# Kernel optimization log

Measured on AMD Instinct MI355X. Metric: run time of the kernel, lower is better.

The kernel has to match this reference:

```python
import jax, jax.numpy as jnp
import numpy as np

N, E, D, H, C = 20000, 320000, 128, 4, 128
NEG_SLOPE = 0.2

def _ln(x, g, b, eps=1e-5):
    mu = x.mean(-1, keepdims=True)
    var = ((x - mu) ** 2).mean(-1, keepdims=True)
    return (x - mu) * jax.lax.rsqrt(var + eps) * g + b

def _gatv2(x, src, dst, Wl, bl, Wr, br, att, b):
    # PyG GATv2Conv, concat=False (mean over heads), dropout off (eval)
    n = x.shape[0]
    xl = (x @ Wl + bl).reshape(n, H, C)   # source transform
    xr = (x @ Wr + br).reshape(n, H, C)   # destination transform
    e = jax.nn.leaky_relu(xl[src] + xr[dst], NEG_SLOPE)      # [E,H,C]
    score = jnp.einsum('ehc,hc->eh', e, att)                 # [E,H]
    m = jax.ops.segment_max(score, dst, num_segments=n)      # per-dst max
    w = jnp.exp(score - m[dst])
    denom = jax.ops.segment_sum(w, dst, num_segments=n)
    alpha = w / (denom[dst] + 1e-16)                         # softmax over incoming edges
    out = jax.ops.segment_sum(alpha[:, :, None] * xl[src], dst, num_segments=n)  # [N,H,C]
    return out.mean(axis=1) + b

def setup_inputs() -> dict:
    key = jax.random.key(0)
    ks = jax.random.split(key, 34)
    s = 1.0 / np.sqrt(D)
    def w(k, shape):
        return jax.random.normal(k, shape, jnp.float32) * s
    inp = {
        'x': jax.random.normal(ks[0], (N, D), jnp.float32),
        'edge_index': jax.random.randint(ks[1], (2, E), 0, N, jnp.int32),
        'W_in': w(ks[2], (D, C)), 'b_in': jnp.zeros((C,), jnp.float32),
        'c1_Wl': w(ks[3], (C, H * C)), 'c1_bl': jnp.zeros((H * C,), jnp.float32),
        'c1_Wr': w(ks[4], (C, H * C)), 'c1_br': jnp.zeros((H * C,), jnp.float32),
        'c1_att': w(ks[5], (H, C)), 'c1_b': jnp.zeros((C,), jnp.float32),
        'ln1_g': jnp.ones((C,), jnp.float32), 'ln1_b': jnp.zeros((C,), jnp.float32),
        'a_Wl': w(ks[6], (C, H * C)), 'a_bl': jnp.zeros((H * C,), jnp.float32),
        'a_Wr': w(ks[7], (C, H * C)), 'a_br': jnp.zeros((H * C,), jnp.float32),
        'a_att': w(ks[8], (H, C)), 'a_b': jnp.zeros((C,), jnp.float32),
        'aln_g': jnp.ones((C,), jnp.float32), 'aln_b': jnp.zeros((C,), jnp.float32),
        'ah_W': w(ks[9], (C, 1)), 'ah_b': jnp.zeros((1,), jnp.float32),
        'k_Wl': w(ks[10], (C, H * C)), 'k_bl': jnp.zeros((H * C,), jnp.float32),
        'k_Wr': w(ks[11], (C, H * C)), 'k_br': jnp.zeros((H * C,), jnp.float32),
        'k_att': w(ks[12], (H, C)), 'k_b': jnp.zeros((C,), jnp.float32),
        'kln_g': jnp.ones((C,), jnp.float32), 'kln_b': jnp.zeros((C,), jnp.float32),
        'kh_W': w(ks[13], (C, 1)), 'kh_b': jnp.zeros((1,), jnp.float32),
    }
    return inp

def reference(x, edge_index, W_in, b_in,
              c1_Wl, c1_bl, c1_Wr, c1_br, c1_att, c1_b, ln1_g, ln1_b,
              a_Wl, a_bl, a_Wr, a_br, a_att, a_b, aln_g, aln_b, ah_W, ah_b,
              k_Wl, k_bl, k_Wr, k_br, k_att, k_b, kln_g, kln_b, kh_W, kh_b):
    n = x.shape[0]
    loops = jnp.arange(n, dtype=edge_index.dtype)
    src = jnp.concatenate([edge_index[0], loops])  # PyG adds self-loops by default
    dst = jnp.concatenate([edge_index[1], loops])
    h = jax.nn.relu(x @ W_in + b_in)
    h_res = _gatv2(h, src, dst, c1_Wl, c1_bl, c1_Wr, c1_br, c1_att, c1_b)
    h = jax.nn.relu(_ln(h + h_res, ln1_g, ln1_b))
    xa = _gatv2(h, src, dst, a_Wl, a_bl, a_Wr, a_br, a_att, a_b)
    xa = jax.nn.relu(_ln(xa + h, aln_g, aln_b))
    action_logits = (xa @ ah_W + ah_b).squeeze(-1)
    xc = _gatv2(h, src, dst, k_Wl, k_bl, k_Wr, k_br, k_att, k_b)
    xc = jax.nn.relu(_ln(xc + h, kln_g, kln_b))
    state_value = xc @ kh_W + kh_b
    return action_logits, state_value
```

## Files before the change

### kernel.cpp

```cpp
#include <hip/hip_runtime.h>
#include <hip/hip_bf16.h>

typedef __hip_bfloat16 bf16;
typedef __attribute__((ext_vector_type(8))) short short8;
typedef __attribute__((ext_vector_type(4))) short short4_t;
typedef __attribute__((ext_vector_type(4))) float float4_t;
typedef __attribute__((ext_vector_type(2))) float float2v;
typedef __attribute__((ext_vector_type(2))) unsigned int uint2v;

__device__ __forceinline__ short f2bs(float f) {
    bf16 b = __float2bfloat16(f);
    return *(short*)&b;
}

template <int CTRL>
__device__ __forceinline__ float dpp_addf(float x) {
    int s = __builtin_amdgcn_update_dpp(
        0, __builtin_bit_cast(int, x), CTRL, 0xf, 0xf, true);
    return x + __builtin_bit_cast(float, s);
}
__device__ __forceinline__ float rowsum16(float x) {
    x = dpp_addf<0xB1>(x);
    x = dpp_addf<0x4E>(x);
    x = dpp_addf<0x141>(x);
    x = dpp_addf<0x140>(x);
    return x;
}

__global__ __launch_bounds__(256) void zero_kernel(int* __restrict__ a, int n) {
    int i = blockIdx.x * 256 + threadIdx.x;
    if (i < n) a[i] = 0;
}

__global__ __launch_bounds__(256) void count_kernel(const int* __restrict__ ei,
                                                    int* __restrict__ cnt, int E, int N) {
    int e = blockIdx.x * 256 + threadIdx.x;
    if (e >= E + N) return;
    int d = (e < E) ? ei[(size_t)E + e] : (e - E);
    atomicAdd(&cnt[d], 1);
}

__global__ __launch_bounds__(1024) void scan_kernel(const int* __restrict__ cnt,
                                                    int* __restrict__ rowptr, int N) {
    __shared__ int ps[1024];
    const int tid = threadIdx.x;
    const int chunk = (N + 1023) / 1024;
    const int base = tid * chunk;
    int s = 0;
    for (int i = 0; i < chunk; ++i) { int j = base + i; if (j < N) s += cnt[j]; }
    ps[tid] = s;
    __syncthreads();
    for (int off = 1; off < 1024; off <<= 1) {
        int v = (tid >= off) ? ps[tid - off] : 0;
        __syncthreads();
        ps[tid] += v;
        __syncthreads();
    }
    int run = (tid == 0) ? 0 : ps[tid - 1];
    for (int i = 0; i < chunk; ++i) {
        int j = base + i;
        if (j < N) { rowptr[j] = run; run += cnt[j]; }
    }
    if (tid == 1023) rowptr[N] = run;
}

__global__ __launch_bounds__(256) void scatter_kernel(const int* __restrict__ ei,
                                                      const int* __restrict__ rowptr,
                                                      int* __restrict__ cursor,
                                                      int* __restrict__ csr_off,
                                                      int E, int N) {
    int e = blockIdx.x * 256 + threadIdx.x;
    if (e >= E + N) return;
    int s, d;
    if (e < E) { s = ei[e]; d = ei[(size_t)E + e]; }
    else       { s = e - E; d = e - E; }
    int pos = atomicAdd(&cursor[d], 1);
    csr_off[rowptr[d] + pos] = s * 4096;
}

__global__ __launch_bounds__(256) void transpose_w_kernel(
        const float* __restrict__ W_in,
        const float* __restrict__ c1_Wl, const float* __restrict__ c1_Wr,
        const float* __restrict__ a_Wl, const float* __restrict__ a_Wr,
        const float* __restrict__ k_Wl, const float* __restrict__ k_Wr,
        bf16* __restrict__ Wt,
        const float* __restrict__ c1_bl, const float* __restrict__ c1_br,
        const float* __restrict__ a_bl, const float* __restrict__ a_br,
        const float* __restrict__ k_bl, const float* __restrict__ k_br,
        float* __restrict__ b1, float* __restrict__ bak) {
    if (blockIdx.z == 7) {
        int flat = blockIdx.y * 16 + blockIdx.x;
        if (flat >= 12) return;
        int i = flat * 256 + threadIdx.x;
        if (i < 1024) {
            b1[i] = (i < 512) ? c1_bl[i] : c1_br[i - 512];
        } else if (i < 3072) {
            int j = i - 1024;
            const float* b = (j < 512) ? a_bl : (j < 1024) ? a_br
                           : (j < 1536) ? k_bl : k_br;
            bak[j] = b[j & 511];
        }
        return;
    }
    __shared__ float tile[32][33];
    const float* src; int nc, drow;
    switch (blockIdx.z) {
        case 0: src = W_in;  nc = 128; drow = 0;    break;
        case 1: src = c1_Wl; nc = 512; drow = 128;  break;
        case 2: src = c1_Wr; nc = 512; drow = 640;  break;
        case 3: src = a_Wl;  nc = 512; drow = 1152; break;
        case 4: src = a_Wr;  nc = 512; drow = 1664; break;
        case 5: src = k_Wl;  nc = 512; drow = 2176; break;
        default: src = k_Wr; nc = 512; drow = 2688; break;
    }
    const int n0 = blockIdx.x * 32;
    if (n0 >= nc) return;
    const int k0 = blockIdx.y * 32;
    const int tx = threadIdx.x & 31, ty = threadIdx.x >> 5;
#pragma unroll
    for (int i = 0; i < 4; ++i)
        tile[ty + i * 8][tx] = src[(size_t)(k0 + ty + i * 8) * nc + n0 + tx];
    __syncthreads();
#pragma unroll
    for (int i = 0; i < 4; ++i)
        Wt[(size_t)(drow + n0 + ty + i * 8) * 128 + k0 + tx] =
            __float2bfloat16(tile[tx][ty + i * 8]);
}

__global__ __launch_bounds__(256, 2) void gemm_mfma_kernel(
        const float* __restrict__ A, const bf16* __restrict__ Ab,
        const bf16* __restrict__ Wt,
        const float* __restrict__ bias,
        float* __restrict__ outF, bf16* __restrict__ outB,
        int M, int ldc, int relu) {
    __shared__ short As[128][136];
    __shared__ short Bs[128][136];
    const int tid = threadIdx.x;
    const int m0 = blockIdx.x * 128;
    const int n0 = blockIdx.y * 128;

    if (Ab) {
        short8 zero8;
#pragma unroll
        for (int q = 0; q < 8; ++q) zero8[q] = 0;
#pragma unroll
        for (int i = 0; i < 8; ++i) {
            int idx = i * 256 + tid;
            int r = idx >> 4, k8 = (idx & 15) * 8;
            int gm = m0 + r;
            short8 s = (gm < M) ? *(const short8*)&Ab[(size_t)gm * 128 + k8] : zero8;
            *(short8*)&As[r][k8] = s;
        }
    } else {
#pragma unroll
        for (int i = 0; i < 16; ++i) {
            int idx = i * 256 + tid;
            int r = idx >> 5, k4 = (idx & 31) * 4;
            int gm = m0 + r;
            float4 v = (gm < M) ? *(const float4*)&A[(size_t)gm * 128 + k4]
                                : make_float4(0.f, 0.f, 0.f, 0.f);
            short4_t s;
            s.x = f2bs(v.x); s.y = f2bs(v.y); s.z = f2bs(v.z); s.w = f2bs(v.w);
            *(short4_t*)&As[r][k4] = s;
        }
    }
#pragma unroll
    for (int i = 0; i < 8; ++i) {
        int idx = i * 256 + tid;
        int nr = idx >> 4, k8 = (idx & 15) * 8;
        *(short8*)&Bs[nr][k8] = *(const short8*)&Wt[(size_t)(n0 + nr) * 128 + k8];
    }
    __syncthreads();

    const int lane = tid & 63;
    const int w = tid >> 6;
    const int wm = (w >> 1) * 64, wn = (w & 1) * 64;
    const int fr = lane & 15;
    const int fq = (lane >> 4) * 8;

    float4_t acc[4][4] = {};
#pragma unroll
    for (int kk = 0; kk < 128; kk += 32) {
        short8 a[4], b[4];
#pragma unroll
        for (int t = 0; t < 4; ++t) a[t] = *(const short8*)&As[wm + t * 16 + fr][kk + fq];
#pragma unroll
        for (int t = 0; t < 4; ++t) b[t] = *(const short8*)&Bs[wn + t * 16 + fr][kk + fq];
#pragma unroll
        for (int ti = 0; ti < 4; ++ti)
#pragma unroll
            for (int tj = 0; tj < 4; ++tj)
                acc[ti][tj] = __builtin_amdgcn_mfma_f32_16x16x32_bf16(
                    a[ti], b[tj], acc[ti][tj], 0, 0, 0);
    }

    const int r0 = (lane >> 4) * 4;
#pragma unroll
    for (int ti = 0; ti < 4; ++ti) {
#pragma unroll
        for (int tj = 0; tj < 4; ++tj) {
            int col = n0 + wn + tj * 16 + fr;
            float bz = bias[col];
#pragma unroll
            for (int r = 0; r < 4; ++r) {
                size_t row = m0 + wm + ti * 16 + r0 + r;
                float v = acc[ti][tj][r] + bz;
                if (relu) v = fmaxf(v, 0.f);
                if (outF) outF[row * ldc + col] = v;
                if (outB) outB[row * ldc + col] = __float2bfloat16(v);
            }
        }
    }
}

__global__ __launch_bounds__(256) void gat_kernel(
        const bf16* __restrict__ xl, const bf16* __restrict__ xr,
        const float* __restrict__ att,
        const int* __restrict__ rowptr, const int* __restrict__ csr_off,
        const float* __restrict__ h_res,
        const float* __restrict__ gbias,
        const float* __restrict__ ln_g, const float* __restrict__ ln_b,
        float* __restrict__ h_out, bf16* __restrict__ h_outb, int N) {
    const int n = blockIdx.x * 4 + (threadIdx.x >> 6);
    if (n >= N) return;
    const int lane = threadIdx.x & 63;
    const int sl = lane & 15;
    const int hc = (lane >> 4) * 128 + sl * 8;

    float2v a2[4], xr2[4];
    {
        const float* ap = att + hc;
        short8 v = *(const short8*)(xr + (size_t)n * 2048 + hc);
        const unsigned int* uv = (const unsigned int*)&v;
#pragma unroll
        for (int j = 0; j < 4; ++j) {
            a2[j].x = ap[2 * j]; a2[j].y = ap[2 * j + 1];
            unsigned u = uv[j];
            xr2[j].x = __uint_as_float(u << 16);
            xr2[j].y = __uint_as_float(u & 0xffff0000u);
        }
    }
    const int rs = rowptr[n], re = rowptr[n + 1];
    const char* xlh = (const char*)xl + (size_t)hc * 2;

    float l = 0.f;
    float2v acc2[4] = {};
    int o0 = csr_off[rs];
    short8 va = *(const short8*)(xlh + o0);
    int o1 = (rs + 1 < re) ? csr_off[rs + 1] : o0;
    short8 vb = *(const short8*)(xlh + o1);
    int o2 = (rs + 2 < re) ? csr_off[rs + 2] : o0;

    for (int e = rs; e < re; ++e) {
        short8 cur = va; va = vb;
        if (e + 2 < re) {
            vb = *(const short8*)(xlh + o2);
            o2 = (e + 3 < re) ? csr_off[e + 3] : o0;
        }
        const unsigned int* uv = (const unsigned int*)&cur;
        float2v pa = {0.f, 0.f}, pb = {0.f, 0.f};
        float2v xs[4];
#pragma unroll
        for (int j = 0; j < 4; ++j) {
            unsigned u = uv[j];
            float2v x;
            x.x = __uint_as_float(u << 16);
            x.y = __uint_as_float(u & 0xffff0000u);
            xs[j] = x;
            float2v t = x + xr2[j];
            float2v ta = __builtin_bit_cast(float2v,
                           __builtin_bit_cast(uint2v, t) & 0x7fffffffu);
            pa = __builtin_elementwise_fma(a2[j], t, pa);
            pb = __builtin_elementwise_fma(a2[j], ta, pb);
        }
        float p = rowsum16(0.6f * (pa.x + pa.y) + 0.4f * (pb.x + pb.y));
        float wv = __expf(fminf(p, 60.f));
        l += wv;
        float2v ws = {wv, wv};
#pragma unroll
        for (int j = 0; j < 4; ++j)
            acc2[j] = __builtin_elementwise_fma(ws, xs[j], acc2[j]);
    }

    float* accf = (float*)acc2;
    const float inv = 0.25f / (l + 1e-16f);
#pragma unroll
    for (int j = 0; j < 8; ++j) accf[j] *= inv;
#pragma unroll
    for (int off = 16; off <= 32; off <<= 1)
#pragma unroll
        for (int j = 0; j < 8; ++j) accf[j] += __shfl_xor(accf[j], off, 64);

    if (lane < 16) {
        const int cb = sl * 8;
        const float* hr = h_res + (size_t)n * 128 + cb;
        float vv[8];
#pragma unroll
        for (int j = 0; j < 8; ++j) vv[j] = accf[j] + gbias[cb + j] + hr[j];
        float t1 = 0.f, t2 = 0.f;
#pragma unroll
        for (int j = 0; j < 8; ++j) { t1 += vv[j]; t2 += vv[j] * vv[j]; }
        const float s1 = rowsum16(t1), s2 = rowsum16(t2);
        const float mu   = s1 * 0.0078125f;
        const float var  = s2 * 0.0078125f - mu * mu;
        const float rstd = rsqrtf(var + 1e-5f);
        float y[8];
#pragma unroll
        for (int j = 0; j < 8; ++j) {
            y[j] = fmaf((vv[j] - mu) * rstd, ln_g[cb + j], ln_b[cb + j]);
            y[j] = fmaxf(y[j], 0.f);
        }
        *(float4*)(h_out + (size_t)n * 128 + cb) = make_float4(y[0], y[1], y[2], y[3]);
        *(float4*)(h_out + (size_t)n * 128 + cb + 4) = make_float4(y[4], y[5], y[6], y[7]);
        short8 yb;
#pragma unroll
        for (int j = 0; j < 8; ++j) yb[j] = f2bs(y[j]);
        *(short8*)(h_outb + (size_t)n * 128 + cb) = yb;
    }
}

__global__ __launch_bounds__(256) void gat2_kernel(
        const bf16* __restrict__ cat,
        const float* __restrict__ a_att, const float* __restrict__ k_att,
        const int* __restrict__ rowptr, const int* __restrict__ csr_off,
        const float* __restrict__ h_res,
        const float* __restrict__ a_gb, const float* __restrict__ k_gb,
        const float* __restrict__ aln_g, const float* __restrict__ aln_b,
        const float* __restrict__ kln_g, const float* __restrict__ kln_b,
        const float* __restrict__ ah_W, const float* __restrict__ ah_b,
        const float* __restrict__ kh_W, const float* __restrict__ kh_b,
        float* __restrict__ out_logits, float* __restrict__ out_value, int N) {
    const int n = blockIdx.x * 4 + (threadIdx.x >> 6);
    if (n >= N) return;
    const int lane = threadIdx.x & 63;
    const int sl = lane & 15;
    const int hc = (lane >> 4) * 128 + sl * 8;

    float2v aa[4], ak[4], xra[4], xrk[4];
    {
        const float* apa = a_att + hc;
        const float* apk = k_att + hc;
        short8 vra = *(const short8*)(cat + (size_t)n * 2048 + 512 + hc);
        short8 vrk = *(const short8*)(cat + (size_t)n * 2048 + 1536 + hc);
        const unsigned int* ua = (const unsigned int*)&vra;
        const unsigned int* uk = (const unsigned int*)&vrk;
#pragma unroll
        for (int j = 0; j < 4; ++j) {
            aa[j].x = apa[2 * j]; aa[j].y = apa[2 * j + 1];
            ak[j].x = apk[2 * j]; ak[j].y = apk[2 * j + 1];
            unsigned u = ua[j];
            xra[j].x = __uint_as_float(u << 16);
            xra[j].y = __uint_as_float(u & 0xffff0000u);
            u = uk[j];
            xrk[j].x = __uint_as_float(u << 16);
            xrk[j].y = __uint_as_float(u & 0xffff0000u);
        }
    }
    const int rs = rowptr[n], re = rowptr[n + 1];
    const char* xlh = (const char*)cat + (size_t)hc * 2;

    float la = 0.f, lk = 0.f;
    float2v acca[4] = {}, acck[4] = {};
    int o0 = csr_off[rs];
    short8 vaa = *(const short8*)(xlh + o0);
    short8 vak = *(const short8*)(xlh + o0 + 2048);
    int o1 = (rs + 1 < re) ? csr_off[rs + 1] : o0;
    short8 vba = *(const short8*)(xlh + o1);
    short8 vbk = *(const short8*)(xlh + o1 + 2048);
    int o2 = (rs + 2 < re) ? csr_off[rs + 2] : o0;

    for (int e = rs; e < re; ++e) {
        short8 ca = vaa, ck = vak;
        vaa = vba; vak = vbk;
        if (e + 2 < re) {
            vba = *(const short8*)(xlh + o2);
            vbk = *(const short8*)(xlh + o2 + 2048);
            o2 = (e + 3 < re) ? csr_off[e + 3] : o0;
        }
        const unsigned int* ua = (const unsigned int*)&ca;
        const unsigned int* uk = (const unsigned int*)&ck;
        float2v paa = {0.f, 0.f}, pba = {0.f, 0.f};
        float2v pak = {0.f, 0.f}, pbk = {0.f, 0.f};
        float2v xsa[4], xsk[4];
#pragma unroll
        for (int j = 0; j < 4; ++j) {
            unsigned u = ua[j];
            float2v x;
            x.x = __uint_as_float(u << 16);
            x.y = __uint_as_float(u & 0xffff0000u);
            xsa[j] = x;
            float2v t = x + xra[j];
            float2v ta = __builtin_bit_cast(float2v,
                           __builtin_bit_cast(uint2v, t) & 0x7fffffffu);
            paa = __builtin_elementwise_fma(aa[j], t, paa);
            pba = __builtin_elementwise_fma(aa[j], ta, pba);

            u = uk[j];
            x.x = __uint_as_float(u << 16);
            x.y = __uint_as_float(u & 0xffff0000u);
            xsk[j] = x;
            t = x + xrk[j];
            ta = __builtin_bit_cast(float2v,
                   __builtin_bit_cast(uint2v, t) & 0x7fffffffu);
            pak = __builtin_elementwise_fma(ak[j], t, pak);
            pbk = __builtin_elementwise_fma(ak[j], ta, pbk);
        }
        float p_a = rowsum16(0.6f * (paa.x + paa.y) + 0.4f * (pba.x + pba.y));
        float p_k = rowsum16(0.6f * (pak.x + pak.y) + 0.4f * (pbk.x + pbk.y));
        float wa = __expf(fminf(p_a, 60.f));
        float wk = __expf(fminf(p_k, 60.f));
        la += wa; lk += wk;
        float2v wsa = {wa, wa}, wsk = {wk, wk};
#pragma unroll
        for (int j = 0; j < 4; ++j) {
            acca[j] = __builtin_elementwise_fma(wsa, xsa[j], acca[j]);
            acck[j] = __builtin_elementwise_fma(wsk, xsk[j], acck[j]);
        }
    }

    float* afa = (float*)acca;
    float* afk = (float*)acck;
    const float inva = 0.25f / (la + 1e-16f);
    const float invk = 0.25f / (lk + 1e-16f);
#pragma unroll
    for (int j = 0; j < 8; ++j) { afa[j] *= inva; afk[j] *= invk; }
#pragma unroll
    for (int off = 16; off <= 32; off <<= 1)
#pragma unroll
        for (int j = 0; j < 8; ++j) {
            afa[j] += __shfl_xor(afa[j], off, 64);
            afk[j] += __shfl_xor(afk[j], off, 64);
        }

    if (lane < 32) {
        const int cb = sl * 8;
        const float* hr = h_res + (size_t)n * 128 + cb;
        float hrv[8];
#pragma unroll
        for (int j = 0; j < 8; ++j) hrv[j] = hr[j];
        if (lane < 16) {
            float vv[8];
#pragma unroll
            for (int j = 0; j < 8; ++j) vv[j] = afa[j] + a_gb[cb + j] + hrv[j];
            float t1 = 0.f, t2 = 0.f;
#pragma unroll
            for (int j = 0; j < 8; ++j) { t1 += vv[j]; t2 += vv[j] * vv[j]; }
            const float s1 = rowsum16(t1), s2 = rowsum16(t2);
            const float mu   = s1 * 0.0078125f;
            const float var  = s2 * 0.0078125f - mu * mu;
            const float rstd = rsqrtf(var + 1e-5f);
            float d = 0.f;
#pragma unroll
            for (int j = 0; j < 8; ++j) {
                float y = fmaf((vv[j] - mu) * rstd, aln_g[cb + j], aln_b[cb + j]);
                d += fmaxf(y, 0.f) * ah_W[cb + j];
            }
            d = rowsum16(d);
            if (sl == 0) out_logits[n] = d + ah_b[0];
        } else {
            float vv[8];
#pragma unroll
            for (int j = 0; j < 8; ++j) vv[j] = afk[j] + k_gb[cb + j] + hrv[j];
            float t1 = 0.f, t2 = 0.f;
#pragma unroll
            for (int j = 0; j < 8; ++j) { t1 += vv[j]; t2 += vv[j] * vv[j]; }
            const float s1 = rowsum16(t1), s2 = rowsum16(t2);
            const float mu   = s1 * 0.0078125f;
            const float var  = s2 * 0.0078125f - mu * mu;
            const float rstd = rsqrtf(var + 1e-5f);
            float d = 0.f;
#pragma unroll
            for (int j = 0; j < 8; ++j) {
                float y = fmaf((vv[j] - mu) * rstd, kln_g[cb + j], kln_b[cb + j]);
                d += fmaxf(y, 0.f) * kh_W[cb + j];
            }
            d = rowsum16(d);
            if (sl == 0) out_value[n] = d + kh_b[0];
        }
    }
}

extern "C" void kernel_launch(void* const* d_in, const int* in_sizes, int n_in,
                              void* d_out, int out_size, void* d_ws, size_t ws_size,
                              hipStream_t stream) {
    const float* x      = (const float*)d_in[0];
    const int*   ei     = (const int*)  d_in[1];
    const float* W_in   = (const float*)d_in[2];
    const float* b_in   = (const float*)d_in[3];
    const float* c1_Wl  = (const float*)d_in[4];
    const float* c1_bl  = (const float*)d_in[5];
    const float* c1_Wr  = (const float*)d_in[6];
    const float* c1_br  = (const float*)d_in[7];
    const float* c1_att = (const float*)d_in[8];
    const float* c1_b   = (const float*)d_in[9];
    const float* ln1_g  = (const float*)d_in[10];
    const float* ln1_b  = (const float*)d_in[11];
    const float* a_Wl   = (const float*)d_in[12];
    const float* a_bl   = (const float*)d_in[13];
    const float* a_Wr   = (const float*)d_in[14];
    const float* a_br   = (const float*)d_in[15];
    const float* a_att  = (const float*)d_in[16];
    const float* a_b    = (const float*)d_in[17];
    const float* aln_g  = (const float*)d_in[18];
    const float* aln_b  = (const float*)d_in[19];
    const float* ah_W   = (const float*)d_in[20];
    const float* ah_b   = (const float*)d_in[21];
    const float* k_Wl   = (const float*)d_in[22];
    const float* k_bl   = (const float*)d_in[23];
    const float* k_Wr   = (const float*)d_in[24];
    const float* k_br   = (const float*)d_in[25];
    const float* k_att  = (const float*)d_in[26];
    const float* k_b    = (const float*)d_in[27];
    const float* kln_g  = (const float*)d_in[28];
    const float* kln_b  = (const float*)d_in[29];
    const float* kh_W   = (const float*)d_in[30];
    const float* kh_b   = (const float*)d_in[31];

    const int N  = in_sizes[0] / 128;
    const int E  = in_sizes[1] / 2;
    const int ET = E + N;
    const int MB = (N + 127) / 128;
    const int Npad = MB * 128;

    char* ws = (char*)d_ws;
    size_t off = 0;
    auto alloc = [&](size_t bytes) -> void* {
        void* p = ws + off;
        off += (bytes + 255) & ~(size_t)255;
        return p;
    };
    int*   rowptr  = (int*)alloc((size_t)(N + 1) * 4);
    int*   cntcur  = (int*)alloc((size_t)2 * N * 4);
    int*   csr_off = (int*)alloc((size_t)ET * 4);
    float* h0      = (float*)alloc((size_t)Npad * 128 * 4);
    bf16*  h0b     = (bf16*)alloc((size_t)Npad * 128 * 2);
    float* h1      = (float*)alloc((size_t)Npad * 128 * 4);
    bf16*  h1b     = (bf16*)alloc((size_t)Npad * 128 * 2);
    bf16*  Wt      = (bf16*)alloc((size_t)3200 * 128 * 2);
    float* b1cat   = (float*)alloc(1024 * 4);
    float* bakcat  = (float*)alloc(2048 * 4);
    bf16*  cat     = (bf16*)alloc((size_t)Npad * 2048 * 2);

    int* cnt    = cntcur;
    int* cursor = cntcur + N;
    const bf16* Wt_in = Wt;
    const bf16* Wt_1  = Wt + 128 * 128;
    const bf16* Wt_ak = Wt + 128 * 128 + 1024 * 128;

    float* out_logits = (float*)d_out;
    float* out_value  = (float*)d_out + N;

    zero_kernel<<<(2 * N + 255) / 256, 256, 0, stream>>>(cntcur, 2 * N);
    count_kernel<<<(ET + 255) / 256, 256, 0, stream>>>(ei, cnt, E, N);
    transpose_w_kernel<<<dim3(16, 4, 8), 256, 0, stream>>>(
        W_in, c1_Wl, c1_Wr, a_Wl, a_Wr, k_Wl, k_Wr, Wt,
        c1_bl, c1_br, a_bl, a_br, k_bl, k_br, b1cat, bakcat);
    scan_kernel<<<1, 1024, 0, stream>>>(cnt, rowptr, N);
    scatter_kernel<<<(ET + 255) / 256, 256, 0, stream>>>(ei, rowptr, cursor, csr_off, E, N);

    gemm_mfma_kernel<<<dim3(MB, 1), 256, 0, stream>>>(x, nullptr, Wt_in, b_in,
                                                      h0, h0b, N, 128, 1);
    gemm_mfma_kernel<<<dim3(MB, 8), 256, 0, stream>>>(nullptr, h0b, Wt_1, b1cat,
                                                      nullptr, cat, Npad, 2048, 0);
    gat_kernel<<<(N + 3) / 4, 256, 0, stream>>>(cat, cat + 512, c1_att, rowptr, csr_off,
                                      h0, c1_b, ln1_g, ln1_b, h1, h1b, N);
    gemm_mfma_kernel<<<dim3(MB, 16), 256, 0, stream>>>(nullptr, h1b, Wt_ak, bakcat,
                                                       nullptr, cat, Npad, 2048, 0);
    gat2_kernel<<<(N + 3) / 4, 256, 0, stream>>>(cat, a_att, k_att, rowptr, csr_off,
                                      h1, a_b, k_b, aln_g, aln_b, kln_g, kln_b,
                                      ah_W, ah_b, kh_W, kh_b,
                                      out_logits, out_value, N);
}
```

Baseline: 411.9 us.

## Merge CSR-build stages into weight-transpose and GEMM launches to cut kernel count

Replaces the zero kernel with hipMemsetAsync. The count pass now runs in the same launch as the weight transpose and bias packing. The prefix scan runs as an extra block inside the first GEMM launch, and the edge scatter runs as extra blocks inside the second GEMM launch. This removes several small kernel launches and their serialization gaps by packing independent work into shared grids. In exchange, the scan is now done by a single 256-thread block rather than 1024 threads, which makes its serial chunk longer and may stretch the tail of the first GEMM launch.

```diff
diff --git a/kernel.cpp b/kernel.cpp
--- a/kernel.cpp
+++ b/kernel.cpp
@@ -27,58 +27,92 @@
     return x;
 }
 
-__global__ __launch_bounds__(256) void zero_kernel(int* __restrict__ a, int n) {
-    int i = blockIdx.x * 256 + threadIdx.x;
-    if (i < n) a[i] = 0;
-}
-
-__global__ __launch_bounds__(256) void count_kernel(const int* __restrict__ ei,
-                                                    int* __restrict__ cnt, int E, int N) {
-    int e = blockIdx.x * 256 + threadIdx.x;
-    if (e >= E + N) return;
-    int d = (e < E) ? ei[(size_t)E + e] : (e - E);
-    atomicAdd(&cnt[d], 1);
-}
-
-__global__ __launch_bounds__(1024) void scan_kernel(const int* __restrict__ cnt,
-                                                    int* __restrict__ rowptr, int N) {
-    __shared__ int ps[1024];
+__device__ __forceinline__ void gemm_body(
+        short (*As)[136], short (*Bs)[136],
+        const float* __restrict__ A, const bf16* __restrict__ Ab,
+        const bf16* __restrict__ Wt, const float* __restrict__ bias,
+        float* __restrict__ outF, bf16* __restrict__ outB,
+        int M, int ldc, int relu, int bx, int by) {
     const int tid = threadIdx.x;
-    const int chunk = (N + 1023) / 1024;
-    const int base = tid * chunk;
-    int s = 0;
-    for (int i = 0; i < chunk; ++i) { int j = base + i; if (j < N) s += cnt[j]; }
-    ps[tid] = s;
+    const int m0 = bx * 128;
+    const int n0 = by * 128;
+
+    if (Ab) {
+        short8 zero8;
+#pragma unroll
+        for (int q = 0; q < 8; ++q) zero8[q] = 0;
+#pragma unroll
+        for (int i = 0; i < 8; ++i) {
+            int idx = i * 256 + tid;
+            int r = idx >> 4, k8 = (idx & 15) * 8;
+            int gm = m0 + r;
+            short8 s = (gm < M) ? *(const short8*)&Ab[(size_t)gm * 128 + k8] : zero8;
+            *(short8*)&As[r][k8] = s;
+        }
+    } else {
+#pragma unroll
+        for (int i = 0; i < 16; ++i) {
+            int idx = i * 256 + tid;
+            int r = idx >> 5, k4 = (idx & 31) * 4;
+            int gm = m0 + r;
+            float4 v = (gm < M) ? *(const float4*)&A[(size_t)gm * 128 + k4]
+                                : make_float4(0.f, 0.f, 0.f, 0.f);
+            short4_t s;
+            s.x = f2bs(v.x); s.y = f2bs(v.y); s.z = f2bs(v.z); s.w = f2bs(v.w);
+            *(short4_t*)&As[r][k4] = s;
+        }
+    }
+#pragma unroll
+    for (int i = 0; i < 8; ++i) {
+        int idx = i * 256 + tid;
+        int nr = idx >> 4, k8 = (idx & 15) * 8;
+        *(short8*)&Bs[nr][k8] = *(const short8*)&Wt[(size_t)(n0 + nr) * 128 + k8];
+    }
     __syncthreads();
-    for (int off = 1; off < 1024; off <<= 1) {
-        int v = (tid >= off) ? ps[tid - off] : 0;
-        __syncthreads();
-        ps[tid] += v;
-        __syncthreads();
-    }
-    int run = (tid == 0) ? 0 : ps[tid - 1];
-    for (int i = 0; i < chunk; ++i) {
-        int j = base + i;
-        if (j < N) { rowptr[j] = run; run += cnt[j]; }
-    }
-    if (tid == 1023) rowptr[N] = run;
-}
-
-__global__ __launch_bounds__(256) void scatter_kernel(const int* __restrict__ ei,
-                                                      const int* __restrict__ rowptr,
-                                                      int* __restrict__ cursor,
-                                                      int* __restrict__ csr_off,
-                                                      int E, int N) {
-    int e = blockIdx.x * 256 + threadIdx.x;
-    if (e >= E + N) return;
-    int s, d;
-    if (e < E) { s = ei[e]; d = ei[(size_t)E + e]; }
-    else       { s = e - E; d = e - E; }
-    int pos = atomicAdd(&cursor[d], 1);
-    csr_off[rowptr[d] + pos] = s * 4096;
-}
-
-__global__ __launch_bounds__(256) void transpose_w_kernel(
+
+    const int lane = tid & 63;
+    const int w = tid >> 6;
+    const int wm = (w >> 1) * 64, wn = (w & 1) * 64;
+    const int fr = lane & 15;
+    const int fq = (lane >> 4) * 8;
+
+    float4_t acc[4][4] = {};
+#pragma unroll
+    for (int kk = 0; kk < 128; kk += 32) {
+        short8 a[4], b[4];
+#pragma unroll
+        for (int t = 0; t < 4; ++t) a[t] = *(const short8*)&As[wm + t * 16 + fr][kk + fq];
+#pragma unroll
+        for (int t = 0; t < 4; ++t) b[t] = *(const short8*)&Bs[wn + t * 16 + fr][kk + fq];
+#pragma unroll
+        for (int ti = 0; ti < 4; ++ti)
+#pragma unroll
+            for (int tj = 0; tj < 4; ++tj)
+                acc[ti][tj] = __builtin_amdgcn_mfma_f32_16x16x32_bf16(
+                    a[ti], b[tj], acc[ti][tj], 0, 0, 0);
+    }
+
+    const int r0 = (lane >> 4) * 4;
+#pragma unroll
+    for (int ti = 0; ti < 4; ++ti) {
+#pragma unroll
+        for (int tj = 0; tj < 4; ++tj) {
+            int col = n0 + wn + tj * 16 + fr;
+            float bz = bias[col];
+#pragma unroll
+            for (int r = 0; r < 4; ++r) {
+                size_t row = m0 + wm + ti * 16 + r0 + r;
+                float v = acc[ti][tj][r] + bz;
+                if (relu) v = fmaxf(v, 0.f);
+                if (outF) outF[row * ldc + col] = v;
+                if (outB) outB[row * ldc + col] = __float2bfloat16(v);
+            }
+        }
+    }
+}
+
+__global__ __launch_bounds__(256) void fused_ct_kernel(
+        const int* __restrict__ ei, int* __restrict__ cnt, int E, int N, int CB,
         const float* __restrict__ W_in,
         const float* __restrict__ c1_Wl, const float* __restrict__ c1_Wr,
         const float* __restrict__ a_Wl, const float* __restrict__ a_Wr,
@@ -88,10 +122,18 @@
         const float* __restrict__ a_bl, const float* __restrict__ a_br,
         const float* __restrict__ k_bl, const float* __restrict__ k_br,
         float* __restrict__ b1, float* __restrict__ bak) {
-    if (blockIdx.z == 7) {
-        int flat = blockIdx.y * 16 + blockIdx.x;
-        if (flat >= 12) return;
-        int i = flat * 256 + threadIdx.x;
+    __shared__ float tile[32][33];
+    const int bid = blockIdx.x;
+    if (bid < CB) {
+        int e = bid * 256 + threadIdx.x;
+        if (e >= E + N) return;
+        int d = (e < E) ? ei[(size_t)E + e] : (e - E);
+        atomicAdd(&cnt[d], 1);
+        return;
+    }
+    int t = bid - CB;
+    if (t >= 448) {
+        int i = (t - 448) * 256 + threadIdx.x;
         if (i < 1024) {
             b1[i] = (i < 512) ? c1_bl[i] : c1_br[i - 512];
         } else if (i < 3072) {
@@ -102,9 +144,11 @@
         }
         return;
     }
-    __shared__ float tile[32][33];
+    const int z = t >> 6, yx = t & 63;
+    const int k0 = (yx >> 4) * 32;
+    const int n0 = (yx & 15) * 32;
     const float* src; int nc, drow;
-    switch (blockIdx.z) {
+    switch (z) {
         case 0: src = W_in;  nc = 128; drow = 0;    break;
         case 1: src = c1_Wl; nc = 512; drow = 128;  break;
         case 2: src = c1_Wr; nc = 512; drow = 640;  break;
@@ -113,9 +157,7 @@
         case 5: src = k_Wl;  nc = 512; drow = 2176; break;
         default: src = k_Wr; nc = 512; drow = 2688; break;
     }
-    const int n0 = blockIdx.x * 32;
     if (n0 >= nc) return;
-    const int k0 = blockIdx.y * 32;
     const int tx = threadIdx.x & 31, ty = threadIdx.x >> 5;
 #pragma unroll
     for (int i = 0; i < 4; ++i)
@@ -127,90 +169,72 @@
             __float2bfloat16(tile[tx][ty + i * 8]);
 }
 
-__global__ __launch_bounds__(256, 2) void gemm_mfma_kernel(
-        const float* __restrict__ A, const bf16* __restrict__ Ab,
-        const bf16* __restrict__ Wt,
+__global__ __launch_bounds__(256, 2) void fused_scan_gemm_kernel(
+        const float* __restrict__ A, const bf16* __restrict__ Wt,
         const float* __restrict__ bias,
         float* __restrict__ outF, bf16* __restrict__ outB,
-        int M, int ldc, int relu) {
+        int M, int ldc, int relu, int GB,
+        const int* __restrict__ cnt, int* __restrict__ rowptr, int Ncnt, int ET) {
     __shared__ short As[128][136];
     __shared__ short Bs[128][136];
+    const int bid = blockIdx.x;
+    if (bid < GB) {
+        gemm_body(As, Bs, A, nullptr, Wt, bias, outF, outB, M, ldc, relu, bid, 0);
+        return;
+    }
+    __shared__ int ps[256];
     const int tid = threadIdx.x;
-    const int m0 = blockIdx.x * 128;
-    const int n0 = blockIdx.y * 128;
-
-    if (Ab) {
-        short8 zero8;
-#pragma unroll
-        for (int q = 0; q < 8; ++q) zero8[q] = 0;
-#pragma unroll
-        for (int i = 0; i < 8; ++i) {
-            int idx = i * 256 + tid;
-            int r = idx >> 4, k8 = (idx & 15) * 8;
-            int gm = m0 + r;
-            short8 s = (gm < M) ? *(const short8*)&Ab[(size_t)gm * 128 + k8] : zero8;
-            *(short8*)&As[r][k8] = s;
-        }
-    } else {
-#pragma unroll
-        for (int i = 0; i < 16; ++i) {
-            int idx = i * 256 + tid;
-            int r = idx >> 5, k4 = (idx & 31) * 4;
-            int gm = m0 + r;
-            float4 v = (gm < M) ? *(const float4*)&A[(size_t)gm * 128 + k4]
-                                : make_float4(0.f, 0.f, 0.f, 0.f);
-            short4_t s;
-            s.x = f2bs(v.x); s.y = f2bs(v.y); s.z = f2bs(v.z); s.w = f2bs(v.w);
-            *(short4_t*)&As[r][k4] = s;
-        }
-    }
-#pragma unroll
-    for (int i = 0; i < 8; ++i) {
-        int idx = i * 256 + tid;
-        int nr = idx >> 4, k8 = (idx & 15) * 8;
-        *(short8*)&Bs[nr][k8] = *(const short8*)&Wt[(size_t)(n0 + nr) * 128 + k8];
-    }
+    const int chunk = (Ncnt + 255) / 256;
+    const int base = tid * chunk;
+    int s = 0;
+    for (int i = 0; i < chunk; ++i) { int j = base + i; if (j < Ncnt) s += cnt[j]; }
+    ps[tid] = s;
     __syncthreads();
-
-    const int lane = tid & 63;
-    const int w = tid >> 6;
-    const int wm = (w >> 1) * 64, wn = (w & 1) * 64;
-    const int fr = lane & 15;
-    const int fq = (lane >> 4) * 8;
-
-    float4_t acc[4][4] = {};
-#pragma unroll
-    for (int kk = 0; kk < 128; kk += 32) {
-        short8 a[4], b[4];
-#pragma unroll
-        for (int t = 0; t < 4; ++t) a[t] = *(const short8*)&As[wm + t * 16 + fr][kk + fq];
-#pragma unroll
-        for (int t = 0; t < 4; ++t) b[t] = *(const short8*)&Bs[wn + t * 16 + fr][kk + fq];
-#pragma unroll
-        for (int ti = 0; ti < 4; ++ti)
-#pragma unroll
-            for (int tj = 0; tj < 4; ++tj)
-                acc[ti][tj] = __builtin_amdgcn_mfma_f32_16x16x32_bf16(
-                    a[ti], b[tj], acc[ti][tj], 0, 0, 0);
-    }
-
-    const int r0 = (lane >> 4) * 4;
-#pragma unroll
-    for (int ti = 0; ti < 4; ++ti) {
-#pragma unroll
-        for (int tj = 0; tj < 4; ++tj) {
-            int col = n0 + wn + tj * 16 + fr;
-            float bz = bias[col];
-#pragma unroll
-            for (int r = 0; r < 4; ++r) {
-                size_t row = m0 + wm + ti * 16 + r0 + r;
-                float v = acc[ti][tj][r] + bz;
-                if (relu) v = fmaxf(v, 0.f);
-                if (outF) outF[row * ldc + col] = v;
-                if (outB) outB[row * ldc + col] = __float2bfloat16(v);
-            }
-        }
-    }
+    for (int off = 1; off < 256; off <<= 1) {
+        int v = (tid >= off) ? ps[tid - off] : 0;
+        __syncthreads();
+        ps[tid] += v;
+        __syncthreads();
+    }
+    int run = (tid == 0) ? 0 : ps[tid - 1];
+    for (int i = 0; i < chunk; ++i) {
+        int j = base + i;
+        if (j < Ncnt) { rowptr[j] = run; run += cnt[j]; }
+    }
+    if (tid == 255) rowptr[Ncnt] = ET;
+}
+
+__global__ __launch_bounds__(256, 2) void fused_scatter_gemm_kernel(
+        const bf16* __restrict__ Ab, const bf16* __restrict__ Wt,
+        const float* __restrict__ bias, bf16* __restrict__ outB,
+        int M, int ldc, int GB, int NBX,
+        const int* __restrict__ ei, const int* __restrict__ rowptr,
+        int* __restrict__ cursor, int* __restrict__ csr_off, int E, int N) {
+    __shared__ short As[128][136];
+    __shared__ short Bs[128][136];
+    const int bid = blockIdx.x;
+    if (bid < GB) {
+        gemm_body(As, Bs, nullptr, Ab, Wt, bias, nullptr, outB, M, ldc, 0,
+                  bid % NBX, bid / NBX);
+        return;
+    }
+    int e = (bid - GB) * 256 + threadIdx.x;
+    if (e >= E + N) return;
+    int s, d;
+    if (e < E) { s = ei[e]; d = ei[(size_t)E + e]; }
+    else       { s = e - E; d = e - E; }
+    int pos = atomicAdd(&cursor[d], 1);
+    csr_off[rowptr[d] + pos] = s * 4096;
+}
+
+__global__ __launch_bounds__(256, 2) void gemm_mfma_kernel(
+        const bf16* __restrict__ Ab, const bf16* __restrict__ Wt,
+        const float* __restrict__ bias, bf16* __restrict__ outB,
+        int M, int ldc) {
+    __shared__ short As[128][136];
+    __shared__ short Bs[128][136];
+    gemm_body(As, Bs, nullptr, Ab, Wt, bias, nullptr, outB, M, ldc, 0,
+              blockIdx.x, blockIdx.y);
 }
 
 __global__ __launch_bounds__(256) void gat_kernel(
@@ -521,6 +545,7 @@
     const int ET = E + N;
     const int MB = (N + 127) / 128;
     const int Npad = MB * 128;
+    const int CB = (ET + 255) / 256;
 
     char* ws = (char*)d_ws;
     size_t off = 0;
@@ -550,22 +575,21 @@
     float* out_logits = (float*)d_out;
     float* out_value  = (float*)d_out + N;
 
-    zero_kernel<<<(2 * N + 255) / 256, 256, 0, stream>>>(cntcur, 2 * N);
-    count_kernel<<<(ET + 255) / 256, 256, 0, stream>>>(ei, cnt, E, N);
-    transpose_w_kernel<<<dim3(16, 4, 8), 256, 0, stream>>>(
+    hipMemsetAsync(cntcur, 0, (size_t)2 * N * 4, stream);
+    fused_ct_kernel<<<CB + 460, 256, 0, stream>>>(
+        ei, cnt, E, N, CB,
         W_in, c1_Wl, c1_Wr, a_Wl, a_Wr, k_Wl, k_Wr, Wt,
         c1_bl, c1_br, a_bl, a_br, k_bl, k_br, b1cat, bakcat);
-    scan_kernel<<<1, 1024, 0, stream>>>(cnt, rowptr, N);
-    scatter_kernel<<<(ET + 255) / 256, 256, 0, stream>>>(ei, rowptr, cursor, csr_off, E, N);
-
-    gemm_mfma_kernel<<<dim3(MB, 1), 256, 0, stream>>>(x, nullptr, Wt_in, b_in,
-                                                      h0, h0b, N, 128, 1);
-    gemm_mfma_kernel<<<dim3(MB, 8), 256, 0, stream>>>(nullptr, h0b, Wt_1, b1cat,
-                                                      nullptr, cat, Npad, 2048, 0);
+    fused_scan_gemm_kernel<<<MB + 1, 256, 0, stream>>>(
+        x, Wt_in, b_in, h0, h0b, N, 128, 1, MB,
+        cnt, rowptr, N, ET);
+    fused_scatter_gemm_kernel<<<MB * 8 + CB, 256, 0, stream>>>(
+        h0b, Wt_1, b1cat, cat, Npad, 2048, MB * 8, MB,
+        ei, rowptr, cursor, csr_off, E, N);
     gat_kernel<<<(N + 3) / 4, 256, 0, stream>>>(cat, cat + 512, c1_att, rowptr, csr_off,
                                       h0, c1_b, ln1_g, ln1_b, h1, h1b, N);
-    gemm_mfma_kernel<<<dim3(MB, 16), 256, 0, stream>>>(nullptr, h1b, Wt_ak, bakcat,
-                                                       nullptr, cat, Npad, 2048, 0);
+    gemm_mfma_kernel<<<dim3(MB, 16), 256, 0, stream>>>(h1b, Wt_ak, bakcat, cat,
+                                                       Npad, 2048);
     gat2_kernel<<<(N + 3) / 4, 256, 0, stream>>>(cat, a_att, k_att, rowptr, csr_off,
                                       h1, a_b, k_b, aln_g, aln_b, kln_g, kln_b,
                                       ah_W, ah_b, kh_W, kh_b,
```

New measurement: 398.2 us. 1.03x faster.
